# Performance work log

Hardware: AMD Instinct MI355X
Metric: run time of the kernel (lower is better)

## Reference

```python
import jax, jax.numpy as jnp
import numpy as np

NUM_EXPERTS = 8
TOP_K = 2
HIDDEN = 1024
INTER = 4096
STD = 0.02


def setup_inputs() -> dict:
    key = jax.random.key(0)
    k0, k1, k2, k3 = jax.random.split(key, 4)
    hidden_states = jax.random.normal(k0, (2, 2048, HIDDEN), dtype=jnp.float32)
    gate_w = jax.random.normal(k1, (NUM_EXPERTS, HIDDEN), dtype=jnp.float32) * (HIDDEN ** -0.5)
    w1 = jax.random.normal(k2, (NUM_EXPERTS, INTER, HIDDEN), dtype=jnp.float32) * STD  # c_fc.weight
    w2 = jax.random.normal(k3, (NUM_EXPERTS, HIDDEN, INTER), dtype=jnp.float32) * STD  # c_proj.weight
    return {"hidden_states": hidden_states, "gate_w": gate_w, "w1": w1, "w2": w2}


def reference(hidden_states, gate_w, w1, w2):
    B, S, H = hidden_states.shape
    x = hidden_states.reshape(-1, H)                      # [T, H]
    T = x.shape[0]
    # ---- routing ----
    router_logits = x @ gate_w.T                          # [T, E]
    top_vals, top_idx = jax.lax.top_k(router_logits, TOP_K)
    router_weights = jax.nn.softmax(top_vals.astype(jnp.float32), axis=-1).astype(x.dtype)
    # dense combine matrix with exactly top_k nonzeros per row (math-equivalent
    # to the sort/grouped-GEMM/scatter-combine pipeline in the torch module)
    combine = jnp.zeros((T, NUM_EXPERTS), x.dtype).at[
        jnp.arange(T)[:, None], top_idx
    ].set(router_weights)                                 # [T, E]
    # ---- experts ----
    h = jax.nn.gelu(jnp.einsum('th,eih->eti', x, w1), approximate=False)  # [E, T, I]
    y = jnp.einsum('eti,ehi->eth', h, w2)                 # [E, T, H]
    out = jnp.einsum('eth,te->th', y, combine)            # weighted combine
    return out.reshape(B, S, H), router_logits
```

## Files before the change

kernel.cpp:

```cpp
#include <hip/hip_runtime.h>

#define T 4096
#define Hdim 1024
#define Idim 4096
#define NE 8
#define OUT0 4194304
#define SPLITK 2

#define SLOT_CAP 9216

#define W1B_OFF 0u
#define W2B_OFF 67108864u
#define XB_OFF  134217728u
#define HB_OFF  142606336u
#define YB_OFF  218103808u
#define META_OFF 255852544u
#define M_COUNTS 0
#define M_CURS   8
#define M_OFFS   16
#define M_TEXP   32
#define M_TSLOT  8224
#define M_STOK   16416
#define M_TWF    25632

typedef short bf16x8 __attribute__((ext_vector_type(8)));
typedef float f32x4  __attribute__((ext_vector_type(4)));

__device__ __forceinline__ unsigned short f2bf(float f) {
    unsigned int b = __float_as_uint(f);
    b += 0x7fffu + ((b >> 16) & 1u);
    return (unsigned short)(b >> 16);
}
__device__ __forceinline__ float bf2f(unsigned short s) {
    return __uint_as_float(((unsigned int)s) << 16);
}

__device__ __forceinline__ void gl_lds16(const void* g, void* l) {
    __builtin_amdgcn_global_load_lds((const __attribute__((address_space(1))) void*)g,
                                     (__attribute__((address_space(3))) void*)l,
                                     16, 0, 0);
}

__global__ void zero_k(int* meta) {
    int i = blockIdx.x * blockDim.x + threadIdx.x;
    if (i < 16) meta[i] = 0;
    if (i < SLOT_CAP) meta[M_STOK + i] = -1;
}

__global__ void cvt_w_k(const float* __restrict__ w1, const float* __restrict__ w2,
                        unsigned short* __restrict__ w1b, unsigned short* __restrict__ w2b,
                        int n4each) {
    int i = blockIdx.x * blockDim.x + threadIdx.x;
    const float4* src; ushort4* dst; int j;
    if (i < n4each) { src = (const float4*)w1; dst = (ushort4*)w1b; j = i; }
    else            { src = (const float4*)w2; dst = (ushort4*)w2b; j = i - n4each; }
    float4 v = src[j];
    ushort4 o;
    o.x = f2bf(v.x); o.y = f2bf(v.y); o.z = f2bf(v.z); o.w = f2bf(v.w);
    dst[j] = o;
}

__global__ void router_k(const float* __restrict__ x, const float* __restrict__ gw,
                         float* __restrict__ logits_out, int* __restrict__ texp,
                         float* __restrict__ twf, int* __restrict__ counts,
                         unsigned short* __restrict__ xb) {
    int wv = threadIdx.x >> 6, lane = threadIdx.x & 63;
    int t = blockIdx.x * 4 + wv;
    const float* xp = x + (size_t)t * Hdim;
    unsigned short* xbp = xb + (size_t)t * Hdim;
    float s[NE];
    #pragma unroll
    for (int e = 0; e < NE; e++) s[e] = 0.f;
    #pragma unroll
    for (int j = 0; j < 16; j++) {
        float xv = xp[lane + 64 * j];
        xbp[lane + 64 * j] = f2bf(xv);
        #pragma unroll
        for (int e = 0; e < NE; e++) s[e] += xv * gw[e * Hdim + lane + 64 * j];
    }
    #pragma unroll
    for (int e = 0; e < NE; e++) {
        #pragma unroll
        for (int off = 32; off > 0; off >>= 1) s[e] += __shfl_xor(s[e], off);
    }
    if (lane == 0) {
        #pragma unroll
        for (int e = 0; e < NE; e++) logits_out[t * NE + e] = s[e];
        int i0 = 0; float v0 = s[0];
        #pragma unroll
        for (int e = 1; e < NE; e++) if (s[e] > v0) { v0 = s[e]; i0 = e; }
        int i1 = -1; float v1 = -3.4e38f;
        #pragma unroll
        for (int e = 0; e < NE; e++) if (e != i0 && s[e] > v1) { v1 = s[e]; i1 = e; }
        float e1 = expf(v1 - v0);
        float inv = 1.f / (1.f + e1);
        texp[2 * t] = i0; texp[2 * t + 1] = i1;
        twf[2 * t] = inv; twf[2 * t + 1] = e1 * inv;
        atomicAdd(&counts[i0], 1);
        atomicAdd(&counts[i1], 1);
    }
}

__global__ void offsets_k(const int* __restrict__ counts, int* __restrict__ offs) {
    if (threadIdx.x == 0 && blockIdx.x == 0) {
        int a = 0; offs[0] = 0;
        for (int e = 0; e < NE; e++) { a += (counts[e] + 127) & ~127; offs[e + 1] = a; }
    }
}

__global__ void assign_k(const int* __restrict__ texp, const int* __restrict__ offs,
                         int* __restrict__ curs, int* __restrict__ stok, int* __restrict__ tslot) {
    int p = blockIdx.x * blockDim.x + threadIdx.x;
    int e = texp[p];
    int slot = offs[e] + atomicAdd(&curs[e], 1);
    stok[slot] = p >> 1;
    tslot[p] = slot;
}

__global__ __launch_bounds__(256) void gemm1_k(
    const unsigned short* __restrict__ xb, const unsigned short* __restrict__ w1b,
    const int* __restrict__ offs, const int* __restrict__ stok,
    unsigned short* __restrict__ hb) {
    __shared__ __align__(16) unsigned short As[128 * 32];
    __shared__ __align__(16) unsigned short Bs[128 * 32];
    const int rt = blockIdx.y, ct = blockIdx.x;
    const int row0 = rt * 128;
    if (row0 >= offs[NE]) return;
    int e = 0;
    #pragma unroll
    for (int q = 1; q < NE; q++) if (offs[q] <= row0) e = q;

    const int tid = threadIdx.x;
    const int lane = tid & 63, wv = tid >> 6;
    const int c0 = wv * 2, c1 = wv * 2 + 1;
    const int rin = lane >> 2, kc = lane & 3;
    const int ar0 = c0 * 16 + rin, ar1 = c1 * 16 + rin;
    int t0 = stok[row0 + ar0]; if (t0 < 0) t0 = 0;
    int t1 = stok[row0 + ar1]; if (t1 < 0) t1 = 0;
    const unsigned short* gA0 = xb + (size_t)t0 * Hdim + kc * 8;
    const unsigned short* gA1 = xb + (size_t)t1 * Hdim + kc * 8;
    const unsigned short* gB0 = w1b + ((size_t)e * Idim + ct * 128 + ar0) * Hdim + kc * 8;
    const unsigned short* gB1 = w1b + ((size_t)e * Idim + ct * 128 + ar1) * Hdim + kc * 8;
    unsigned short* lA0 = As + c0 * 512; unsigned short* lA1 = As + c1 * 512;
    unsigned short* lB0 = Bs + c0 * 512; unsigned short* lB1 = Bs + c1 * 512;

    f32x4 acc[4][4] = {};
    const int mrow = (wv & 1) * 64, ncol = (wv >> 1) * 64;
    const int fr = lane & 15, qd = lane >> 4;

    for (int kk = 0; kk < Hdim; kk += 32) {
        gl_lds16(gA0 + kk, lA0);
        gl_lds16(gA1 + kk, lA1);
        gl_lds16(gB0 + kk, lB0);
        gl_lds16(gB1 + kk, lB1);
        __syncthreads();
        bf16x8 af[4], bff[4];
        #pragma unroll
        for (int mi = 0; mi < 4; mi++) af[mi]  = *(const bf16x8*)&As[(mrow + mi * 16 + fr) * 32 + qd * 8];
        #pragma unroll
        for (int ni = 0; ni < 4; ni++) bff[ni] = *(const bf16x8*)&Bs[(ncol + ni * 16 + fr) * 32 + qd * 8];
        #pragma unroll
        for (int mi = 0; mi < 4; mi++)
            #pragma unroll
            for (int ni = 0; ni < 4; ni++)
                acc[mi][ni] = __builtin_amdgcn_mfma_f32_16x16x32_bf16(af[mi], bff[ni], acc[mi][ni], 0, 0, 0);
        __syncthreads();
    }
    #pragma unroll
    for (int mi = 0; mi < 4; mi++) {
        #pragma unroll
        for (int ni = 0; ni < 4; ni++) {
            #pragma unroll
            for (int r = 0; r < 4; r++) {
                int row = row0 + mrow + mi * 16 + qd * 4 + r;
                int col = ct * 128 + ncol + ni * 16 + fr;
                float v = acc[mi][ni][r];
                float u = v * (1.f + 0.044715f * v * v);
                float g = v / (1.f + __expf(-1.5957691216f * u));
                hb[(size_t)row * Idim + col] = f2bf(g);
            }
        }
    }
}

__global__ __launch_bounds__(256) void gemm2_k(
    const unsigned short* __restrict__ hb, const unsigned short* __restrict__ w2b,
    const int* __restrict__ offs, unsigned short* __restrict__ y16) {
    __shared__ __align__(16) unsigned short As[128 * 32];
    __shared__ __align__(16) unsigned short Bs[128 * 32];
    const int rt = blockIdx.y, ct = blockIdx.x, kz = blockIdx.z;
    const int row0 = rt * 128;
    if (row0 >= offs[NE]) return;
    int e = 0;
    #pragma unroll
    for (int q = 1; q < NE; q++) if (offs[q] <= row0) e = q;

    const int tid = threadIdx.x;
    const int lane = tid & 63, wv = tid >> 6;
    const int c0 = wv * 2, c1 = wv * 2 + 1;
    const int rin = lane >> 2, kc = lane & 3;
    const int ar0 = c0 * 16 + rin, ar1 = c1 * 16 + rin;
    const unsigned short* gA0 = hb + (size_t)(row0 + ar0) * Idim + kc * 8;
    const unsigned short* gA1 = hb + (size_t)(row0 + ar1) * Idim + kc * 8;
    const unsigned short* gB0 = w2b + ((size_t)e * Hdim + ct * 128 + ar0) * Idim + kc * 8;
    const unsigned short* gB1 = w2b + ((size_t)e * Hdim + ct * 128 + ar1) * Idim + kc * 8;
    unsigned short* lA0 = As + c0 * 512; unsigned short* lA1 = As + c1 * 512;
    unsigned short* lB0 = Bs + c0 * 512; unsigned short* lB1 = Bs + c1 * 512;

    f32x4 acc[4][4] = {};
    const int mrow = (wv & 1) * 64, ncol = (wv >> 1) * 64;
    const int fr = lane & 15, qd = lane >> 4;

    const int k0 = kz * (Idim / SPLITK), k1 = k0 + (Idim / SPLITK);
    for (int kk = k0; kk < k1; kk += 32) {
        gl_lds16(gA0 + kk, lA0);
        gl_lds16(gA1 + kk, lA1);
        gl_lds16(gB0 + kk, lB0);
        gl_lds16(gB1 + kk, lB1);
        __syncthreads();
        bf16x8 af[4], bff[4];
        #pragma unroll
        for (int mi = 0; mi < 4; mi++) af[mi]  = *(const bf16x8*)&As[(mrow + mi * 16 + fr) * 32 + qd * 8];
        #pragma unroll
        for (int ni = 0; ni < 4; ni++) bff[ni] = *(const bf16x8*)&Bs[(ncol + ni * 16 + fr) * 32 + qd * 8];
        #pragma unroll
        for (int mi = 0; mi < 4; mi++)
            #pragma unroll
            for (int ni = 0; ni < 4; ni++)
                acc[mi][ni] = __builtin_amdgcn_mfma_f32_16x16x32_bf16(af[mi], bff[ni], acc[mi][ni], 0, 0, 0);
        __syncthreads();
    }
    unsigned short* yk = y16 + (size_t)kz * SLOT_CAP * Hdim;
    #pragma unroll
    for (int mi = 0; mi < 4; mi++) {
        #pragma unroll
        for (int ni = 0; ni < 4; ni++) {
            #pragma unroll
            for (int r = 0; r < 4; r++) {
                int row = row0 + mrow + mi * 16 + qd * 4 + r;
                int col = ct * 128 + ncol + ni * 16 + fr;
                yk[(size_t)row * Hdim + col] = f2bf(acc[mi][ni][r]);
            }
        }
    }
}

__global__ void combine_k(const unsigned short* __restrict__ y16, const int* __restrict__ tslot,
                          const float* __restrict__ twf, float* __restrict__ out) {
    int i = blockIdx.x * blockDim.x + threadIdx.x;
    int t = i >> 7, rem = i & 127;
    int s0 = tslot[2 * t], s1 = tslot[2 * t + 1];
    float w0 = twf[2 * t], w1 = twf[2 * t + 1];
    const uint4* y0 = (const uint4*)(y16);
    const uint4* y1 = (const uint4*)(y16 + (size_t)SLOT_CAP * Hdim);
    uint4 a0 = y0[(size_t)s0 * 128 + rem];
    uint4 a1 = y1[(size_t)s0 * 128 + rem];
    uint4 b0 = y0[(size_t)s1 * 128 + rem];
    uint4 b1 = y1[(size_t)s1 * 128 + rem];
    float o[8];
    #pragma unroll
    for (int j = 0; j < 4; j++) {
        unsigned int ua0 = ((const unsigned int*)&a0)[j], ua1 = ((const unsigned int*)&a1)[j];
        unsigned int ub0 = ((const unsigned int*)&b0)[j], ub1 = ((const unsigned int*)&b1)[j];
        float alo = bf2f((unsigned short)ua0) + bf2f((unsigned short)ua1);
        float ahi = bf2f((unsigned short)(ua0 >> 16)) + bf2f((unsigned short)(ua1 >> 16));
        float blo = bf2f((unsigned short)ub0) + bf2f((unsigned short)ub1);
        float bhi = bf2f((unsigned short)(ub0 >> 16)) + bf2f((unsigned short)(ub1 >> 16));
        o[2 * j]     = w0 * alo + w1 * blo;
        o[2 * j + 1] = w0 * ahi + w1 * bhi;
    }
    float4* out4 = (float4*)out;
    out4[2 * i]     = make_float4(o[0], o[1], o[2], o[3]);
    out4[2 * i + 1] = make_float4(o[4], o[5], o[6], o[7]);
}

extern "C" void kernel_launch(void* const* d_in, const int* in_sizes, int n_in,
                              void* d_out, int out_size, void* d_ws, size_t ws_size,
                              hipStream_t stream) {
    const float* x  = (const float*)d_in[0];
    const float* gw = (const float*)d_in[1];
    const float* w1 = (const float*)d_in[2];
    const float* w2 = (const float*)d_in[3];
    float* out = (float*)d_out;

    char* ws = (char*)d_ws;
    unsigned short* w1b = (unsigned short*)(ws + W1B_OFF);
    unsigned short* w2b = (unsigned short*)(ws + W2B_OFF);
    unsigned short* xb  = (unsigned short*)(ws + XB_OFF);
    unsigned short* hb  = (unsigned short*)(ws + HB_OFF);
    unsigned short* y16 = (unsigned short*)(ws + YB_OFF);
    int*            meta = (int*)(ws + META_OFF);
    int* counts = meta + M_COUNTS;
    int* curs   = meta + M_CURS;
    int* offs   = meta + M_OFFS;
    int* texp   = meta + M_TEXP;
    int* tslot  = meta + M_TSLOT;
    int* stok   = meta + M_STOK;
    float* twf  = (float*)(meta + M_TWF);

    zero_k<<<36, 256, 0, stream>>>(meta);
    cvt_w_k<<<65536, 256, 0, stream>>>(w1, w2, w1b, w2b, NE * Idim * Hdim / 4);
    router_k<<<T / 4, 256, 0, stream>>>(x, gw, out + OUT0, texp, twf, counts, xb);
    offsets_k<<<1, 64, 0, stream>>>(counts, offs);
    assign_k<<<32, 256, 0, stream>>>(texp, offs, curs, stok, tslot);
    gemm1_k<<<dim3(Idim / 128, SLOT_CAP / 128), 256, 0, stream>>>(xb, w1b, offs, stok, hb);
    gemm2_k<<<dim3(Hdim / 128, SLOT_CAP / 128, SPLITK), 256, 0, stream>>>(hb, w2b, offs, y16);
    combine_k<<<T * Hdim / 8 / 256, 256, 0, stream>>>(y16, tslot, twf, out);
}
```

Before: 676.3 us.

## Double K tile to 64 with XOR-swizzled LDS and remap gemm2 block order

Both expert GEMMs now load a 128x64 K-tile per barrier pair instead of 128x32, halving the number of sync points per K sweep. The LDS layout is XOR-swizzled by row so the wider rows avoid bank conflicts on the fragment reads. gemm2 switches to a 1D grid whose index is decoded so blocks sharing a row tile and k-split are grouped, with row tiles spread in strides of nine across the low bits, to change L2 locality and placement across XCDs. LDS use doubles to 32 KB per block, which may lower occupancy.

```diff
diff --git a/kernel.cpp b/kernel.cpp
--- a/kernel.cpp
+++ b/kernel.cpp
@@ -6,6 +6,7 @@
 #define NE 8
 #define OUT0 4194304
 #define SPLITK 2
+#define BK 64
 
 #define SLOT_CAP 9216
 
@@ -121,8 +122,8 @@
     const unsigned short* __restrict__ xb, const unsigned short* __restrict__ w1b,
     const int* __restrict__ offs, const int* __restrict__ stok,
     unsigned short* __restrict__ hb) {
-    __shared__ __align__(16) unsigned short As[128 * 32];
-    __shared__ __align__(16) unsigned short Bs[128 * 32];
+    __shared__ __align__(16) unsigned short As[128 * BK];
+    __shared__ __align__(16) unsigned short Bs[128 * BK];
     const int rt = blockIdx.y, ct = blockIdx.x;
     const int row0 = rt * 128;
     if (row0 >= offs[NE]) return;
@@ -132,38 +133,47 @@
 
     const int tid = threadIdx.x;
     const int lane = tid & 63, wv = tid >> 6;
-    const int c0 = wv * 2, c1 = wv * 2 + 1;
-    const int rin = lane >> 2, kc = lane & 3;
-    const int ar0 = c0 * 16 + rin, ar1 = c1 * 16 + rin;
-    int t0 = stok[row0 + ar0]; if (t0 < 0) t0 = 0;
-    int t1 = stok[row0 + ar1]; if (t1 < 0) t1 = 0;
-    const unsigned short* gA0 = xb + (size_t)t0 * Hdim + kc * 8;
-    const unsigned short* gA1 = xb + (size_t)t1 * Hdim + kc * 8;
-    const unsigned short* gB0 = w1b + ((size_t)e * Idim + ct * 128 + ar0) * Hdim + kc * 8;
-    const unsigned short* gB1 = w1b + ((size_t)e * Idim + ct * 128 + ar1) * Hdim + kc * 8;
-    unsigned short* lA0 = As + c0 * 512; unsigned short* lA1 = As + c1 * 512;
-    unsigned short* lB0 = Bs + c0 * 512; unsigned short* lB1 = Bs + c1 * 512;
+    const int srow = lane >> 3;
+    const int schunk = (lane & 7) ^ srow;
+
+    const unsigned short* gA[4]; const unsigned short* gB[4];
+    unsigned short *lA[4], *lB[4];
+    #pragma unroll
+    for (int i = 0; i < 4; i++) {
+        int r = wv * 32 + i * 8 + srow;
+        int t = stok[row0 + r]; if (t < 0) t = 0;
+        gA[i] = xb + (size_t)t * Hdim + schunk * 8;
+        gB[i] = w1b + ((size_t)e * Idim + ct * 128 + r) * Hdim + schunk * 8;
+        lA[i] = As + (wv * 32 + i * 8) * BK;
+        lB[i] = Bs + (wv * 32 + i * 8) * BK;
+    }
 
     f32x4 acc[4][4] = {};
     const int mrow = (wv & 1) * 64, ncol = (wv >> 1) * 64;
     const int fr = lane & 15, qd = lane >> 4;
 
-    for (int kk = 0; kk < Hdim; kk += 32) {
-        gl_lds16(gA0 + kk, lA0);
-        gl_lds16(gA1 + kk, lA1);
-        gl_lds16(gB0 + kk, lB0);
-        gl_lds16(gB1 + kk, lB1);
+    for (int kk = 0; kk < Hdim; kk += BK) {
+        #pragma unroll
+        for (int i = 0; i < 4; i++) {
+            gl_lds16(gA[i] + kk, lA[i]);
+            gl_lds16(gB[i] + kk, lB[i]);
+        }
         __syncthreads();
-        bf16x8 af[4], bff[4];
-        #pragma unroll
-        for (int mi = 0; mi < 4; mi++) af[mi]  = *(const bf16x8*)&As[(mrow + mi * 16 + fr) * 32 + qd * 8];
-        #pragma unroll
-        for (int ni = 0; ni < 4; ni++) bff[ni] = *(const bf16x8*)&Bs[(ncol + ni * 16 + fr) * 32 + qd * 8];
-        #pragma unroll
-        for (int mi = 0; mi < 4; mi++)
+        #pragma unroll
+        for (int ko = 0; ko < 2; ko++) {
+            bf16x8 af[4], bff[4];
+            #pragma unroll
+            for (int mi = 0; mi < 4; mi++)
+                af[mi]  = *(const bf16x8*)&As[(mrow + mi * 16 + fr) * BK + ((((ko << 2) | qd) ^ (fr & 7)) << 3)];
             #pragma unroll
             for (int ni = 0; ni < 4; ni++)
-                acc[mi][ni] = __builtin_amdgcn_mfma_f32_16x16x32_bf16(af[mi], bff[ni], acc[mi][ni], 0, 0, 0);
+                bff[ni] = *(const bf16x8*)&Bs[(ncol + ni * 16 + fr) * BK + ((((ko << 2) | qd) ^ (fr & 7)) << 3)];
+            #pragma unroll
+            for (int mi = 0; mi < 4; mi++)
+                #pragma unroll
+                for (int ni = 0; ni < 4; ni++)
+                    acc[mi][ni] = __builtin_amdgcn_mfma_f32_16x16x32_bf16(af[mi], bff[ni], acc[mi][ni], 0, 0, 0);
+        }
         __syncthreads();
     }
     #pragma unroll
@@ -186,9 +196,15 @@
 __global__ __launch_bounds__(256) void gemm2_k(
     const unsigned short* __restrict__ hb, const unsigned short* __restrict__ w2b,
     const int* __restrict__ offs, unsigned short* __restrict__ y16) {
-    __shared__ __align__(16) unsigned short As[128 * 32];
-    __shared__ __align__(16) unsigned short Bs[128 * 32];
-    const int rt = blockIdx.y, ct = blockIdx.x, kz = blockIdx.z;
+    __shared__ __align__(16) unsigned short As[128 * BK];
+    __shared__ __align__(16) unsigned short Bs[128 * BK];
+    const int id = blockIdx.x;
+    const int k8 = id & 7;
+    const int j  = id >> 3;
+    const int ct = j & 7;
+    const int j8 = j >> 3;
+    const int rtL = j8 % 9, kz = j8 / 9;
+    const int rt = k8 * 9 + rtL;
     const int row0 = rt * 128;
     if (row0 >= offs[NE]) return;
     int e = 0;
@@ -197,37 +213,47 @@
 
     const int tid = threadIdx.x;
     const int lane = tid & 63, wv = tid >> 6;
-    const int c0 = wv * 2, c1 = wv * 2 + 1;
-    const int rin = lane >> 2, kc = lane & 3;
-    const int ar0 = c0 * 16 + rin, ar1 = c1 * 16 + rin;
-    const unsigned short* gA0 = hb + (size_t)(row0 + ar0) * Idim + kc * 8;
-    const unsigned short* gA1 = hb + (size_t)(row0 + ar1) * Idim + kc * 8;
-    const unsigned short* gB0 = w2b + ((size_t)e * Hdim + ct * 128 + ar0) * Idim + kc * 8;
-    const unsigned short* gB1 = w2b + ((size_t)e * Hdim + ct * 128 + ar1) * Idim + kc * 8;
-    unsigned short* lA0 = As + c0 * 512; unsigned short* lA1 = As + c1 * 512;
-    unsigned short* lB0 = Bs + c0 * 512; unsigned short* lB1 = Bs + c1 * 512;
+    const int srow = lane >> 3;
+    const int schunk = (lane & 7) ^ srow;
+
+    const unsigned short* gA[4]; const unsigned short* gB[4];
+    unsigned short *lA[4], *lB[4];
+    #pragma unroll
+    for (int i = 0; i < 4; i++) {
+        int r = wv * 32 + i * 8 + srow;
+        gA[i] = hb + (size_t)(row0 + r) * Idim + schunk * 8;
+        gB[i] = w2b + ((size_t)e * Hdim + ct * 128 + r) * Idim + schunk * 8;
+        lA[i] = As + (wv * 32 + i * 8) * BK;
+        lB[i] = Bs + (wv * 32 + i * 8) * BK;
+    }
 
     f32x4 acc[4][4] = {};
     const int mrow = (wv & 1) * 64, ncol = (wv >> 1) * 64;
     const int fr = lane & 15, qd = lane >> 4;
 
     const int k0 = kz * (Idim / SPLITK), k1 = k0 + (Idim / SPLITK);
-    for (int kk = k0; kk < k1; kk += 32) {
-        gl_lds16(gA0 + kk, lA0);
-        gl_lds16(gA1 + kk, lA1);
-        gl_lds16(gB0 + kk, lB0);
-        gl_lds16(gB1 + kk, lB1);
+    for (int kk = k0; kk < k1; kk += BK) {
+        #pragma unroll
+        for (int i = 0; i < 4; i++) {
+            gl_lds16(gA[i] + kk, lA[i]);
+            gl_lds16(gB[i] + kk, lB[i]);
+        }
         __syncthreads();
-        bf16x8 af[4], bff[4];
-        #pragma unroll
-        for (int mi = 0; mi < 4; mi++) af[mi]  = *(const bf16x8*)&As[(mrow + mi * 16 + fr) * 32 + qd * 8];
-        #pragma unroll
-        for (int ni = 0; ni < 4; ni++) bff[ni] = *(const bf16x8*)&Bs[(ncol + ni * 16 + fr) * 32 + qd * 8];
-        #pragma unroll
-        for (int mi = 0; mi < 4; mi++)
+        #pragma unroll
+        for (int ko = 0; ko < 2; ko++) {
+            bf16x8 af[4], bff[4];
+            #pragma unroll
+            for (int mi = 0; mi < 4; mi++)
+                af[mi]  = *(const bf16x8*)&As[(mrow + mi * 16 + fr) * BK + ((((ko << 2) | qd) ^ (fr & 7)) << 3)];
             #pragma unroll
             for (int ni = 0; ni < 4; ni++)
-                acc[mi][ni] = __builtin_amdgcn_mfma_f32_16x16x32_bf16(af[mi], bff[ni], acc[mi][ni], 0, 0, 0);
+                bff[ni] = *(const bf16x8*)&Bs[(ncol + ni * 16 + fr) * BK + ((((ko << 2) | qd) ^ (fr & 7)) << 3)];
+            #pragma unroll
+            for (int mi = 0; mi < 4; mi++)
+                #pragma unroll
+                for (int ni = 0; ni < 4; ni++)
+                    acc[mi][ni] = __builtin_amdgcn_mfma_f32_16x16x32_bf16(af[mi], bff[ni], acc[mi][ni], 0, 0, 0);
+        }
         __syncthreads();
     }
     unsigned short* yk = y16 + (size_t)kz * SLOT_CAP * Hdim;
@@ -304,6 +330,6 @@
     offsets_k<<<1, 64, 0, stream>>>(counts, offs);
     assign_k<<<32, 256, 0, stream>>>(texp, offs, curs, stok, tslot);
     gemm1_k<<<dim3(Idim / 128, SLOT_CAP / 128), 256, 0, stream>>>(xb, w1b, offs, stok, hb);
-    gemm2_k<<<dim3(Hdim / 128, SLOT_CAP / 128, SPLITK), 256, 0, stream>>>(hb, w2b, offs, y16);
+    gemm2_k<<<(Hdim / 128) * (SLOT_CAP / 128) * SPLITK, 256, 0, stream>>>(hb, w2b, offs, y16);
     combine_k<<<T * Hdim / 8 / 256, 256, 0, stream>>>(y16, tslot, twf, out);
 }
```

After: 672.3 us. About the same (-0.6%).
